# Optimization experiments

Hardware: AMD Instinct MI355X
Metric: run time of the kernel (lower is better)

Reference implementation:

```python
import jax, jax.numpy as jnp
import numpy as np

N_NODES = 50000
N_EDGES = 1600000
IN_FEAT = 128
OUT_FEAT = 128
NUM_RELS = 40


def setup_inputs() -> dict:
    key = jax.random.key(0)
    ks = jax.random.split(key, 8)
    h = jax.random.normal(ks[0], (N_NODES, IN_FEAT), dtype=jnp.float32)
    # Linear(in_feat, out_feat, bias=False): weight shape [out, in]
    W = jax.random.normal(ks[1], (OUT_FEAT, IN_FEAT), dtype=jnp.float32) / np.sqrt(IN_FEAT)
    # attn_fc: Linear(2*out_feat, 1, bias=False): weight shape [1, 2*out]
    attn_w = jax.random.normal(ks[2], (1, 2 * OUT_FEAT), dtype=jnp.float32) / np.sqrt(2 * OUT_FEAT)
    # Embedding(num_rels, 1, padding_idx=0): row 0 zeroed
    rel_emb = jax.random.normal(ks[3], (NUM_RELS, 1), dtype=jnp.float32)
    rel_emb = rel_emb.at[0].set(0.0)
    stdv = 1.0 / np.sqrt(OUT_FEAT)
    bias_w = jax.random.uniform(ks[4], (OUT_FEAT,), minval=-stdv, maxval=stdv, dtype=jnp.float32)
    src = jax.random.randint(ks[5], (N_EDGES,), 0, N_NODES, dtype=jnp.int32)
    dst = jax.random.randint(ks[6], (N_EDGES,), 0, N_NODES, dtype=jnp.int32)
    etype = jax.random.randint(ks[7], (N_EDGES,), 0, NUM_RELS, dtype=jnp.int32)
    return {"h": h, "W": W, "attn_w": attn_w, "rel_emb": rel_emb,
            "bias_w": bias_w, "src": src, "dst": dst, "etype": etype}


def reference(h, W, attn_w, rel_emb, bias_w, src, dst, etype):
    n = h.shape[0]
    out_feat = W.shape[0]
    # z = weight(h)
    z = h @ W.T  # [N, out]
    # attn_fc(cat(z_src, z_dst)) = z_src @ w1 + z_dst @ w2 (decompose to per-node scores)
    w1 = attn_w[0, :out_feat]
    w2 = attn_w[0, out_feat:]
    s_src = z @ w1  # [N]
    s_dst = z @ w2  # [N]
    e = jax.nn.leaky_relu(s_src[src] + s_dst[dst], negative_slope=0.01)  # [E]
    rel_alpha = rel_emb[etype, 0]  # [E]
    # per-dst-node softmax over incoming edges (ragged mailbox softmax)
    m = jax.ops.segment_max(e, dst, num_segments=n)
    num = jnp.exp(e - m[dst])
    den = jax.ops.segment_sum(num, dst, num_segments=n)
    alpha = num / den[dst]
    # h_dst = sum_e rel_alpha_e * alpha_e * z[src_e]
    w_e = (rel_alpha * alpha)[:, None]  # [E,1]
    h_agg = jax.ops.segment_sum(w_e * z[src], dst, num_segments=n)  # [N, out]
    # RGCNLayer.forward: + bias; no BN/activation for GATLayer; dropout = eval identity
    return h_agg + bias_w
```

## Files before the change

kernel.cpp:

```cpp
#include <hip/hip_runtime.h>
#include <hip/hip_fp16.h>

#define NFEAT 128
#define NBUK_MAX 1024
#define HB 256
#define BCAP_L 4096
#define HPAD 136

typedef __attribute__((ext_vector_type(8))) _Float16 f16x8;
typedef __attribute__((ext_vector_type(4))) float f32x4;

__global__ __launch_bounds__(256) void k_gemm_mfma(
    const float* __restrict__ h, const float* __restrict__ W,
    const float* __restrict__ attn_w,
    __half* __restrict__ zh, float* __restrict__ s1, float* __restrict__ s2, int n)
{
    __shared__ _Float16 hsh[64 * HPAD];
    __shared__ _Float16 wsh[128 * HPAD];
    const int tid = threadIdx.x;
    const int wv = tid >> 6, lane = tid & 63;
    const int nodeBase = blockIdx.x * 64;

    {
        const float4* W4 = reinterpret_cast<const float4*>(W);
        for (int t = tid; t < 128 * 32; t += 256) {
            int r = t >> 5, c4 = t & 31;
            float4 v = W4[t];
            _Float16* d = &wsh[r * HPAD + c4 * 4];
            d[0] = (_Float16)v.x; d[1] = (_Float16)v.y;
            d[2] = (_Float16)v.z; d[3] = (_Float16)v.w;
        }
    }
    {
        const float4* h4 = reinterpret_cast<const float4*>(h);
        for (int t = tid; t < 64 * 32; t += 256) {
            int r = t >> 5, c4 = t & 31;
            int node = nodeBase + r;
            float4 v = (node < n) ? h4[(size_t)node * 32 + c4]
                                  : make_float4(0.f, 0.f, 0.f, 0.f);
            _Float16* d = &hsh[r * HPAD + c4 * 4];
            d[0] = (_Float16)v.x; d[1] = (_Float16)v.y;
            d[2] = (_Float16)v.z; d[3] = (_Float16)v.w;
        }
    }
    __syncthreads();

    const int arow = lane & 15;
    const int kgrp = lane >> 4;
    f32x4 acc[8];
#pragma unroll
    for (int t = 0; t < 8; ++t) acc[t] = (f32x4){0.f, 0.f, 0.f, 0.f};

#pragma unroll
    for (int k0 = 0; k0 < 128; k0 += 32) {
        f16x8 a = *reinterpret_cast<const f16x8*>(
            &hsh[(wv * 16 + arow) * HPAD + k0 + kgrp * 8]);
#pragma unroll
        for (int nt = 0; nt < 8; ++nt) {
            f16x8 b = *reinterpret_cast<const f16x8*>(
                &wsh[(nt * 16 + arow) * HPAD + k0 + kgrp * 8]);
            acc[nt] = __builtin_amdgcn_mfma_f32_16x16x32_f16(a, b, acc[nt], 0, 0, 0);
        }
    }

    {
        float pr1[4] = {0.f, 0.f, 0.f, 0.f}, pr2[4] = {0.f, 0.f, 0.f, 0.f};
#pragma unroll
        for (int nt = 0; nt < 8; ++nt) {
            float w1v = attn_w[nt * 16 + arow];
            float w2v = attn_w[128 + nt * 16 + arow];
#pragma unroll
            for (int r = 0; r < 4; ++r) {
                pr1[r] += acc[nt][r] * w1v;
                pr2[r] += acc[nt][r] * w2v;
            }
        }
#pragma unroll
        for (int off = 1; off < 16; off <<= 1) {
#pragma unroll
            for (int r = 0; r < 4; ++r) {
                pr1[r] += __shfl_xor(pr1[r], off);
                pr2[r] += __shfl_xor(pr2[r], off);
            }
        }
        if (arow == 0) {
#pragma unroll
            for (int r = 0; r < 4; ++r) {
                int node = nodeBase + wv * 16 + kgrp * 4 + r;
                if (node < n) { s1[node] = pr1[r]; s2[node] = pr2[r]; }
            }
        }
    }

    _Float16* zout = &hsh[wv * 16 * HPAD];
#pragma unroll
    for (int nt = 0; nt < 8; ++nt)
#pragma unroll
        for (int r = 0; r < 4; ++r)
            zout[(kgrp * 4 + r) * HPAD + nt * 16 + arow] = (_Float16)acc[nt][r];

    {
        int node = nodeBase + wv * 16 + arow;
        if (node < n) {
            const uint4* zsrc = reinterpret_cast<const uint4*>(&zout[arow * HPAD + kgrp * 32]);
            uint4* zdst = reinterpret_cast<uint4*>(zh) + (size_t)node * 16 + kgrp * 4;
            uint4 v0 = zsrc[0], v1 = zsrc[1], v2 = zsrc[2], v3 = zsrc[3];
            zdst[0] = v0; zdst[1] = v1; zdst[2] = v2; zdst[3] = v3;
        }
    }
}

__global__ __launch_bounds__(256) void k_hist(const int* __restrict__ dst,
                                              int* __restrict__ hist,
                                              int e, int nbuk, int epb)
{
    __shared__ int lh[NBUK_MAX];
    const int b = blockIdx.x, tid = threadIdx.x;
    for (int k = tid; k < nbuk; k += 256) lh[k] = 0;
    __syncthreads();
    const int beg = b * epb, end = min(e, beg + epb);
    for (int i = beg + tid; i < end; i += 256)
        atomicAdd(&lh[dst[i] >> 6], 1);
    __syncthreads();
    for (int k = tid; k < nbuk; k += 256)
        hist[b * nbuk + k] = lh[k];
}

__global__ __launch_bounds__(256) void k_scan_blocks(const int* __restrict__ hist,
                                                     int* __restrict__ base,
                                                     int* __restrict__ bucket_tot, int nbuk)
{
    __shared__ int wsum[4];
    const int k = blockIdx.x, tid = threadIdx.x;
    int v = hist[tid * nbuk + k];
    int lane = tid & 63, wave = tid >> 6;
    int x = v;
#pragma unroll
    for (int off = 1; off < 64; off <<= 1) {
        int t = __shfl_up(x, off);
        if (lane >= off) x += t;
    }
    if (lane == 63) wsum[wave] = x;
    __syncthreads();
    int wb = 0;
    for (int w = 0; w < wave; ++w) wb += wsum[w];
    base[tid * nbuk + k] = wb + x - v;
    if (tid == 255) bucket_tot[k] = wb + x;
}

__global__ __launch_bounds__(256) void k_scan_buckets(const int* __restrict__ bucket_tot,
                                                      int* __restrict__ bucket_base,
                                                      int* __restrict__ row_start,
                                                      int n, int nbuk)
{
    __shared__ int wsum[4];
    const int tid = threadIdx.x;
    const int C = (nbuk + 255) / 256;
    const int base_i = tid * C;
    int vals[8];
    int s = 0;
#pragma unroll
    for (int j = 0; j < 8; ++j) {
        int v = 0;
        if (j < C) {
            int idx = base_i + j;
            if (idx < nbuk) v = bucket_tot[idx];
        }
        vals[j] = v; s += v;
    }
    int lane = tid & 63, wave = tid >> 6;
    int x = s;
#pragma unroll
    for (int off = 1; off < 64; off <<= 1) {
        int t = __shfl_up(x, off);
        if (lane >= off) x += t;
    }
    if (lane == 63) wsum[wave] = x;
    __syncthreads();
    int wb = 0;
    for (int w = 0; w < wave; ++w) wb += wsum[w];
    int ex = wb + x - s;
#pragma unroll
    for (int j = 0; j < 8; ++j) {
        if (j < C) {
            int idx = base_i + j;
            if (idx < nbuk) bucket_base[idx] = ex;
            ex += vals[j];
        }
    }
    if (tid == 255) row_start[n] = ex;
}

__global__ __launch_bounds__(256) void k_sctr(
    const int* __restrict__ src, const int* __restrict__ dst, const int* __restrict__ etype,
    const int* __restrict__ base, const int* __restrict__ bucket_base,
    unsigned int* __restrict__ bucket_store, int e, int nbuk, int epb)
{
    __shared__ int cur[NBUK_MAX];
    const int b = blockIdx.x, tid = threadIdx.x;
    for (int k = tid; k < nbuk; k += 256)
        cur[k] = base[b * nbuk + k] + bucket_base[k];
    __syncthreads();
    const int beg = b * epb, end = min(e, beg + epb);
    for (int i = beg + tid; i < end; i += 256) {
        int d = dst[i];
        int pos = atomicAdd(&cur[d >> 6], 1);
        bucket_store[pos] =
            (unsigned int)src[i] | ((unsigned int)etype[i] << 16) | ((unsigned int)(d & 63) << 22);
    }
}

__global__ __launch_bounds__(256) void k_place(
    const unsigned int* __restrict__ bucket_store, const int* __restrict__ bucket_tot,
    const int* __restrict__ bucket_base,
    int* __restrict__ row_start, unsigned int* __restrict__ edge_list, int n)
{
    __shared__ unsigned int est[BCAP_L];
    __shared__ int cnt64[64];
    const int b = blockIdx.x;
    const int tid = threadIdx.x;
    const int cnt = min(bucket_tot[b], BCAP_L);
    const int base = bucket_base[b];

    if (tid < 64) cnt64[tid] = 0;
    for (int j = tid; j < cnt; j += 256)
        est[j] = bucket_store[(size_t)base + j];
    __syncthreads();
    for (int j = tid; j < cnt; j += 256)
        atomicAdd(&cnt64[est[j] >> 22], 1);
    __syncthreads();
    if (tid < 64) {
        int v = cnt64[tid];
        int x = v;
#pragma unroll
        for (int off = 1; off < 64; off <<= 1) {
            int t = __shfl_up(x, off);
            if (tid >= off) x += t;
        }
        int node = (b << 6) + tid;
        if (node < n) row_start[node] = base + x - v;
        cnt64[tid] = x - v;
    }
    __syncthreads();
    for (int j = tid; j < cnt; j += 256) {
        unsigned int pk = est[j];
        int pos = base + atomicAdd(&cnt64[pk >> 22], 1);
        edge_list[pos] = pk & 0x3FFFFFu;
    }
}

__global__ __launch_bounds__(256) void k_aggregate(
    const __half* __restrict__ zh, const float* __restrict__ s1, const float* __restrict__ s2,
    const float* __restrict__ rel_emb, const float* __restrict__ bias,
    const int* __restrict__ row_start, const unsigned int* __restrict__ edge_list,
    float* __restrict__ out, int n)
{
    __shared__ uint2 lds_ws[4][64];
    const int wv   = threadIdx.x >> 6;
    const int lane = threadIdx.x & 63;
    const int node = blockIdx.x * 4 + wv;
    if (node >= n) return;

    const int beg = row_start[node];
    const int end = row_start[node + 1];
    const int deg = end - beg;
    const int quad = lane >> 4;
    const int q    = lane & 15;

    float acc[8];
#pragma unroll
    for (int j = 0; j < 8; ++j) acc[j] = 0.f;
    const uint4* z4 = reinterpret_cast<const uint4*>(zh);

    if (deg > 0) {
        const float s2n = s2[node];

        if (deg <= 64) {
            unsigned int pk = 0;
            float ev = -3.4e38f;
            const bool has = lane < deg;
            if (has) {
                pk = edge_list[beg + lane];
                ev = s1[pk & 0xFFFFu] + s2n;
                ev = ev > 0.f ? ev : 0.01f * ev;
            }
            float m = ev;
#pragma unroll
            for (int off = 32; off > 0; off >>= 1)
                m = fmaxf(m, __shfl_xor(m, off));
            float p = has ? __expf(ev - m) : 0.f;
            float den = p;
#pragma unroll
            for (int off = 32; off > 0; off >>= 1)
                den += __shfl_xor(den, off);
            const float inv = 1.f / den;
            const int   src_i = has ? (int)(pk & 0xFFFFu) : 0;
            const float wgt   = has ? rel_emb[pk >> 16] * p * inv : 0.f;

            int jb = 0;
            for (; jb + 16 <= deg; jb += 16) {
                const int j0 = jb + quad;
                int   sA = __shfl(src_i, j0),      sB = __shfl(src_i, j0 + 4);
                int   sC = __shfl(src_i, j0 + 8),  sD = __shfl(src_i, j0 + 12);
                float wA = __shfl(wgt, j0),        wB = __shfl(wgt, j0 + 4);
                float wC = __shfl(wgt, j0 + 8),    wD = __shfl(wgt, j0 + 12);
                uint4 vA = z4[(size_t)sA * 16 + q];
                uint4 vB = z4[(size_t)sB * 16 + q];
                uint4 vC = z4[(size_t)sC * 16 + q];
                uint4 vD = z4[(size_t)sD * 16 + q];
                const __half* hA = reinterpret_cast<const __half*>(&vA);
                const __half* hB = reinterpret_cast<const __half*>(&vB);
                const __half* hC = reinterpret_cast<const __half*>(&vC);
                const __half* hD = reinterpret_cast<const __half*>(&vD);
#pragma unroll
                for (int k2 = 0; k2 < 8; ++k2) {
                    acc[k2] += wA * __half2float(hA[k2]);
                    acc[k2] += wB * __half2float(hB[k2]);
                    acc[k2] += wC * __half2float(hC[k2]);
                    acc[k2] += wD * __half2float(hD[k2]);
                }
            }
            for (; jb < deg; jb += 4) {
                const int j = jb + quad;
                int   sj = __shfl(src_i, j);
                float wj = __shfl(wgt, j);
                uint4 zv = z4[(size_t)sj * 16 + q];
                const __half* hp = reinterpret_cast<const __half*>(&zv);
#pragma unroll
                for (int k2 = 0; k2 < 8; ++k2)
                    acc[k2] += wj * __half2float(hp[k2]);
            }
        } else {
            float mymax = -3.4e38f;
            for (int k = beg + lane; k < end; k += 64) {
                unsigned int pk = edge_list[k];
                float ev = s1[pk & 0xFFFFu] + s2n;
                ev = ev > 0.f ? ev : 0.01f * ev;
                mymax = fmaxf(mymax, ev);
            }
#pragma unroll
            for (int off = 32; off > 0; off >>= 1)
                mymax = fmaxf(mymax, __shfl_xor(mymax, off));
            float mysum = 0.f;
            for (int k = beg + lane; k < end; k += 64) {
                unsigned int pk = edge_list[k];
                float ev = s1[pk & 0xFFFFu] + s2n;
                ev = ev > 0.f ? ev : 0.01f * ev;
                mysum += __expf(ev - mymax);
            }
#pragma unroll
            for (int off = 32; off > 0; off >>= 1)
                mysum += __shfl_xor(mysum, off);
            const float inv = 1.f / mysum;

            for (int cb = beg; cb < end; cb += 64) {
                int k = cb + lane;
                if (k < end) {
                    unsigned int pk = edge_list[k];
                    int s = pk & 0xFFFFu;
                    float ev = s1[s] + s2n;
                    ev = ev > 0.f ? ev : 0.01f * ev;
                    lds_ws[wv][lane] = make_uint2((unsigned)s,
                        __float_as_uint(rel_emb[pk >> 16] * __expf(ev - mymax) * inv));
                }
                int cnt = min(64, end - cb);
#pragma unroll 2
                for (int j = quad; j < cnt; j += 4) {
                    uint2 t = lds_ws[wv][j];
                    float w = __uint_as_float(t.y);
                    uint4 zv = z4[(size_t)t.x * 16 + q];
                    const __half* hp = reinterpret_cast<const __half*>(&zv);
#pragma unroll
                    for (int k2 = 0; k2 < 8; ++k2)
                        acc[k2] += w * __half2float(hp[k2]);
                }
            }
        }
#pragma unroll
        for (int j = 0; j < 8; ++j) {
            acc[j] += __shfl_xor(acc[j], 16);
            acc[j] += __shfl_xor(acc[j], 32);
        }
    }

    if (quad == 0) {
        const float4* b4 = reinterpret_cast<const float4*>(bias);
        float4 b0 = b4[q * 2], b1 = b4[q * 2 + 1];
        float4* o4 = reinterpret_cast<float4*>(out);
        o4[(size_t)node * 32 + q * 2] =
            make_float4(acc[0] + b0.x, acc[1] + b0.y, acc[2] + b0.z, acc[3] + b0.w);
        o4[(size_t)node * 32 + q * 2 + 1] =
            make_float4(acc[4] + b1.x, acc[5] + b1.y, acc[6] + b1.z, acc[7] + b1.w);
    }
}

extern "C" void kernel_launch(void* const* d_in, const int* in_sizes, int n_in,
                              void* d_out, int out_size, void* d_ws, size_t ws_size,
                              hipStream_t stream) {
    const float* h      = (const float*)d_in[0];
    const float* W      = (const float*)d_in[1];
    const float* attn_w = (const float*)d_in[2];
    const float* rel    = (const float*)d_in[3];
    const float* bias   = (const float*)d_in[4];
    const int*   src    = (const int*)d_in[5];
    const int*   dst    = (const int*)d_in[6];
    const int*   etype  = (const int*)d_in[7];
    const int n = in_sizes[0] / NFEAT;
    const int e = in_sizes[5];
    const int nbuk = (n + 63) / 64;
    const int epb = (e + HB - 1) / HB;
    float* out = (float*)d_out;

    char* p = (char*)d_ws;
    __half* zh = (__half*)p;               p += (size_t)n * NFEAT * 2;
    float* s1 = (float*)p;                 p += (size_t)n * 4;
    float* s2 = (float*)p;                 p += (size_t)n * 4;
    int* row_start = (int*)p;              p += (size_t)(n + 1) * 4;
    int* hist       = (int*)p;             p += (size_t)HB * nbuk * 4;
    int* base       = (int*)p;             p += (size_t)HB * nbuk * 4;
    int* bucket_tot = (int*)p;             p += (size_t)nbuk * 4;
    int* bucket_base= (int*)p;             p += (size_t)nbuk * 4;
    unsigned int* edge_list    = (unsigned int*)p;  p += (size_t)e * 4;
    unsigned int* bucket_store = (unsigned int*)p;  p += (size_t)e * 4;

    k_gemm_mfma<<<(n + 63) / 64, 256, 0, stream>>>(h, W, attn_w, zh, s1, s2, n);
    k_hist<<<HB, 256, 0, stream>>>(dst, hist, e, nbuk, epb);
    k_scan_blocks<<<nbuk, 256, 0, stream>>>(hist, base, bucket_tot, nbuk);
    k_scan_buckets<<<1, 256, 0, stream>>>(bucket_tot, bucket_base, row_start, n, nbuk);
    k_sctr<<<HB, 256, 0, stream>>>(src, dst, etype, base, bucket_base, bucket_store, e, nbuk, epb);
    k_place<<<nbuk, 256, 0, stream>>>(bucket_store, bucket_tot, bucket_base, row_start, edge_list, n);
    k_aggregate<<<(n + 3) / 4, 256, 0, stream>>>(zh, s1, s2, rel, bias, row_start, edge_list, out, n);
}
```

Baseline: 128.7 us.

## Stage scatter in shared memory to coalesce bucket_store writes

```diff
diff --git a/kernel.cpp b/kernel.cpp
--- a/kernel.cpp
+++ b/kernel.cpp
@@ -4,6 +4,7 @@
 #define NFEAT 128
 #define NBUK_MAX 1024
 #define HB 256
+#define EPB_MAX 6272
 #define BCAP_L 4096
 #define HPAD 136
 
@@ -196,18 +197,75 @@
     const int* __restrict__ base, const int* __restrict__ bucket_base,
     unsigned int* __restrict__ bucket_store, int e, int nbuk, int epb)
 {
-    __shared__ int cur[NBUK_MAX];
+    __shared__ unsigned int est[EPB_MAX];
+    __shared__ unsigned short bkt[EPB_MAX];
+    __shared__ int lcnt[NBUK_MAX];
+    __shared__ int gbase[NBUK_MAX];
+    __shared__ int lcur[NBUK_MAX];
+    __shared__ int wsum[4];
+
     const int b = blockIdx.x, tid = threadIdx.x;
-    for (int k = tid; k < nbuk; k += 256)
-        cur[k] = base[b * nbuk + k] + bucket_base[k];
-    __syncthreads();
     const int beg = b * epb, end = min(e, beg + epb);
+    const int cnt = end - beg;
+
+    for (int k = tid; k < nbuk; k += 256) lcnt[k] = 0;
+    __syncthreads();
+    for (int i = beg + tid; i < end; i += 256)
+        atomicAdd(&lcnt[dst[i] >> 6], 1);
+    __syncthreads();
+
+    const int C = (nbuk + 255) / 256;
+    const int bi = tid * C;
+    int vals[4];
+    int s = 0;
+#pragma unroll
+    for (int j = 0; j < 4; ++j) {
+        int v = 0;
+        if (j < C) {
+            int idx = bi + j;
+            if (idx < nbuk) v = lcnt[idx];
+        }
+        vals[j] = v; s += v;
+    }
+    const int lane = tid & 63, wv = tid >> 6;
+    int x = s;
+#pragma unroll
+    for (int off = 1; off < 64; off <<= 1) {
+        int t = __shfl_up(x, off);
+        if (lane >= off) x += t;
+    }
+    if (lane == 63) wsum[wv] = x;
+    __syncthreads();
+    int wb = 0;
+    for (int w = 0; w < wv; ++w) wb += wsum[w];
+    int ex = wb + x - s;
+#pragma unroll
+    for (int j = 0; j < 4; ++j) {
+        if (j < C) {
+            int idx = bi + j;
+            if (idx < nbuk) {
+                lcnt[idx] = ex;
+                lcur[idx] = ex;
+                gbase[idx] = bucket_base[idx] + base[b * nbuk + idx] - ex;
+                ex += vals[j];
+            }
+        }
+    }
+    __syncthreads();
+
     for (int i = beg + tid; i < end; i += 256) {
         int d = dst[i];
-        int pos = atomicAdd(&cur[d >> 6], 1);
-        bucket_store[pos] =
+        int k = d >> 6;
+        unsigned int word =
             (unsigned int)src[i] | ((unsigned int)etype[i] << 16) | ((unsigned int)(d & 63) << 22);
-    }
+        int pos = atomicAdd(&lcur[k], 1);
+        est[pos] = word;
+        bkt[pos] = (unsigned short)k;
+    }
+    __syncthreads();
+
+    for (int j = tid; j < cnt; j += 256)
+        bucket_store[gbase[bkt[j]] + j] = est[j];
 }
 
 __global__ __launch_bounds__(256) void k_place(
```

Measured after the change: 124.2 us. 1.04x faster.
